# Kernel tuning notes

Hardware: AMD Instinct MI355X
Metric: run time of the kernel (lower is better)

Reference implementation:

```python
import jax, jax.numpy as jnp
import numpy as np
import math

D_MODEL = 2048
N_HEADS = 32
N_KV_HEADS = 8
HEAD_DIM = D_MODEL // N_HEADS  # 64
GROUPS = N_HEADS // N_KV_HEADS  # 4
WINDOW = 512


def setup_inputs() -> dict:
    key = jax.random.key(0)
    k0, k1, k2, k3, k4 = jax.random.split(key, 5)
    B, T = 1, 2048
    scale = 0.02
    return {
        "hidden_states": jax.random.normal(k0, (B, T, D_MODEL), dtype=jnp.float32),
        "Wq": jax.random.normal(k1, (D_MODEL, D_MODEL), dtype=jnp.float32) * scale,
        "Wk": jax.random.normal(k2, (N_KV_HEADS * HEAD_DIM, D_MODEL), dtype=jnp.float32) * scale,
        "Wv": jax.random.normal(k3, (N_KV_HEADS * HEAD_DIM, D_MODEL), dtype=jnp.float32) * scale,
        "Wo": jax.random.normal(k4, (D_MODEL, D_MODEL), dtype=jnp.float32) * scale,
    }


def _rope_tables(T, dim):
    # matches RotaryEmbedding: inv_freq over even indices, emb = cat(freqs, freqs)
    inv_freq = 1.0 / (10000.0 ** (jnp.arange(0, dim, 2, dtype=jnp.float32) / dim))
    freqs = jnp.arange(T, dtype=jnp.float32)[:, None] * inv_freq[None, :]  # [T, dim/2]
    emb = jnp.concatenate([freqs, freqs], axis=-1)  # [T, dim]
    return jnp.cos(emb), jnp.sin(emb)


def _rotate_half(x):
    d = x.shape[-1] // 2
    return jnp.concatenate([-x[..., d:], x[..., :d]], axis=-1)


def reference(hidden_states, Wq, Wk, Wv, Wo):
    B, T, _ = hidden_states.shape
    # projections (torch Linear: y = x @ W^T)
    q = (hidden_states @ Wq.T).reshape(B, T, N_HEADS, HEAD_DIM).transpose(0, 2, 1, 3)      # [B,H,T,D]
    k = (hidden_states @ Wk.T).reshape(B, T, N_KV_HEADS, HEAD_DIM).transpose(0, 2, 1, 3)   # [B,Hkv,T,D]
    v = (hidden_states @ Wv.T).reshape(B, T, N_KV_HEADS, HEAD_DIM).transpose(0, 2, 1, 3)
    # RoPE (cos/sin broadcast [T,D] over [B,H,T,D])
    cos, sin = _rope_tables(T, HEAD_DIM)
    q = q * cos + _rotate_half(q) * sin
    k = k * cos + _rotate_half(k) * sin
    # GQA: expand KV heads
    k = jnp.repeat(k, GROUPS, axis=1)  # [B,H,T,D]
    v = jnp.repeat(v, GROUPS, axis=1)
    scores = jnp.einsum('bhqd,bhkd->bhqk', q, k) / math.sqrt(HEAD_DIM)  # [B,H,T,T]
    if WINDOW < T:
        i = jnp.arange(T)[:, None]
        j = jnp.arange(T)[None, :]
        # row i keeps columns [max(0,i-W/2), min(T,i+W/2)) — same as the torch loop
        allowed = (j >= i - WINDOW // 2) & (j < i + WINDOW // 2)
        scores = jnp.where(allowed, scores, -jnp.inf)
    w = jax.nn.softmax(scores, axis=-1)
    out = jnp.einsum('bhqk,bhkd->bhqd', w, v)  # [B,H,T,D]
    out = out.transpose(0, 2, 1, 3).reshape(B, T, D_MODEL)
    return out @ Wo.T
```

## Files before the change

kernel.cpp:

```cpp
#include <hip/hip_runtime.h>
#include <math.h>

#define TLEN 2048
#define DMODEL 2048
#define NHEADS 32
#define NKV 8
#define HDIM 64
#define KVDIM 512
#define WHALF 256

typedef short shortx8 __attribute__((ext_vector_type(8)));
typedef float floatx4 __attribute__((ext_vector_type(4)));
typedef unsigned int uint32;

__device__ __forceinline__ unsigned short f2bf_rne(float x) {
    union { float f; uint32 u; } v; v.f = x;
    uint32 r = v.u + 0x7FFFu + ((v.u >> 16) & 1u);
    return (unsigned short)(r >> 16);
}

#define GL16(g, l)                                                              \
    __builtin_amdgcn_global_load_lds(                                           \
        (const __attribute__((address_space(1))) unsigned int*)(g),             \
        (__attribute__((address_space(3))) unsigned int*)(l), 16, 0, 0)

__global__ __launch_bounds__(256) void convert_inputs(const float* __restrict__ hs,
                                                      const float* __restrict__ Wq,
                                                      const float* __restrict__ Wk,
                                                      const float* __restrict__ Wv,
                                                      const float* __restrict__ Wo,
                                                      unsigned short* __restrict__ hsb,
                                                      unsigned short* __restrict__ Wcat,
                                                      unsigned short* __restrict__ Wob) {
    int b = blockIdx.x;
    const float* src; unsigned short* dst;
    if (b < 512)       { src = hs; dst = hsb; }
    else if (b < 1024) { src = Wq; dst = Wcat;                           b -= 512; }
    else if (b < 1152) { src = Wk; dst = Wcat + (size_t)2048 * DMODEL;   b -= 1024; }
    else if (b < 1280) { src = Wv; dst = Wcat + (size_t)2560 * DMODEL;   b -= 1152; }
    else               { src = Wo; dst = Wob;                            b -= 1280; }
    size_t base = (size_t)b * 8192 + threadIdx.x * 4;
#pragma unroll
    for (int it = 0; it < 8; ++it) {
        size_t off = base + (size_t)it * 1024;
        float4 v = *(const float4*)(src + off);
        short4 p;
        p.x = (short)f2bf_rne(v.x); p.y = (short)f2bf_rne(v.y);
        p.z = (short)f2bf_rne(v.z); p.w = (short)f2bf_rne(v.w);
        *(short4*)(dst + off) = p;
    }
}

__global__ __launch_bounds__(256) void gemm_qkv(const unsigned short* __restrict__ hsb,
                                                const unsigned short* __restrict__ Wcat,
                                                unsigned short* __restrict__ Qo,
                                                unsigned short* __restrict__ Ko,
                                                unsigned short* __restrict__ Vo) {
    __shared__ short Ah[128][128];
    __shared__ short Bh[64][128];

    const int bnx = blockIdx.x;
    int mode, coff;
    if (bnx < 32)      { mode = 0; coff = bnx * 64; }
    else if (bnx < 40) { mode = 1; coff = (bnx - 32) * 64; }
    else               { mode = 2; coff = (bnx - 40) * 64; }
    const unsigned short* Bbase = Wcat + (size_t)bnx * 64 * DMODEL;

    const int bm = blockIdx.y * 128;
    const int tid = threadIdx.x;
    const int w = tid >> 6, lane = tid & 63;
    const int wA = w * 32, wB = w * 16;
    const int lr = lane & 15, quad = lane >> 4;
    const int r4 = lane >> 4;

    const unsigned short* Ag[4];
    const unsigned short* Bg[4];
#pragma unroll
    for (int gm = 0; gm < 4; ++gm) {
        const int cof = ((lane & 15) ^ r4 ^ (gm << 2)) * 8;
        Ag[gm] = hsb   + (size_t)(bm + wA + 4 * gm + r4) * DMODEL + cof;
        Bg[gm] = Bbase + (size_t)(wB + 4 * gm + r4) * DMODEL + cof;
    }

    floatx4 acc[2][4];
#pragma unroll
    for (int i = 0; i < 2; ++i)
#pragma unroll
        for (int j = 0; j < 4; ++j) acc[i][j] = (floatx4)0.0f;

    for (int k0 = 0; k0 < DMODEL; k0 += 128) {
        __syncthreads();
#pragma unroll
        for (int q = 0; q < 2; ++q)
#pragma unroll
            for (int gm = 0; gm < 4; ++gm)
                GL16(Ag[gm] + (size_t)(16 * q) * DMODEL + k0, &Ah[wA + 16 * q + 4 * gm][0]);
#pragma unroll
        for (int gm = 0; gm < 4; ++gm)
            GL16(Bg[gm] + k0, &Bh[wB + 4 * gm][0]);
        __syncthreads();

#pragma unroll
        for (int s = 0; s < 4; ++s) {
            const int cs = ((s * 4 + quad) ^ lr) * 8;
            shortx8 a0 = *(shortx8*)&Ah[wA + lr][cs];
            shortx8 a1 = *(shortx8*)&Ah[wA + 16 + lr][cs];
            shortx8 bf[4];
#pragma unroll
            for (int j = 0; j < 4; ++j) bf[j] = *(shortx8*)&Bh[j * 16 + lr][cs];
#pragma unroll
            for (int j = 0; j < 4; ++j)
                acc[0][j] = __builtin_amdgcn_mfma_f32_16x16x32_bf16(a0, bf[j], acc[0][j], 0, 0, 0);
#pragma unroll
            for (int j = 0; j < 4; ++j)
                acc[1][j] = __builtin_amdgcn_mfma_f32_16x16x32_bf16(a1, bf[j], acc[1][j], 0, 0, 0);
        }
    }

    if (mode != 2) {
#pragma unroll
        for (int j = 0; j < 2; ++j) {
            float fr = exp2f(-(float)(j * 16 + lr) * (13.2877123795494f / 32.0f));
#pragma unroll
            for (int i = 0; i < 2; ++i) {
                const int row0 = bm + wA + i * 16 + quad * 4;
#pragma unroll
                for (int r = 0; r < 4; ++r) {
                    float s, c;
                    sincosf((float)(row0 + r) * fr, &s, &c);
                    float x1 = acc[i][j][r], x2 = acc[i][j + 2][r];
                    acc[i][j][r]     = x1 * c - x2 * s;
                    acc[i][j + 2][r] = x2 * c + x1 * s;
                }
            }
        }
    }

#pragma unroll
    for (int i = 0; i < 2; ++i) {
        const int row0 = bm + wA + i * 16 + quad * 4;
        if (mode == 0) {
#pragma unroll
            for (int j = 0; j < 4; ++j) {
                int col = coff + j * 16 + lr;
#pragma unroll
                for (int r = 0; r < 4; ++r)
                    Qo[(size_t)(row0 + r) * DMODEL + col] = f2bf_rne(0.125f * acc[i][j][r]);
            }
        } else if (mode == 1) {
#pragma unroll
            for (int j = 0; j < 4; ++j) {
                int col = coff + j * 16 + lr;
#pragma unroll
                for (int r = 0; r < 4; ++r)
                    Ko[(size_t)(row0 + r) * KVDIM + col] = f2bf_rne(acc[i][j][r]);
            }
        } else {
#pragma unroll
            for (int j = 0; j < 4; ++j) {
                int col = coff + j * 16 + lr;
                short4 pk;
                pk.x = (short)f2bf_rne(acc[i][j][0]);
                pk.y = (short)f2bf_rne(acc[i][j][1]);
                pk.z = (short)f2bf_rne(acc[i][j][2]);
                pk.w = (short)f2bf_rne(acc[i][j][3]);
                *(short4*)&Vo[(size_t)col * TLEN + row0] = pk;
            }
        }
    }
}

__global__ __launch_bounds__(512) void attn_mfma(const unsigned short* __restrict__ Qb,
                                                 const unsigned short* __restrict__ Kb,
                                                 const unsigned short* __restrict__ Vt,
                                                 unsigned short* __restrict__ Ab) {
    __shared__ short Qs[128][64];
    __shared__ short Ks[2][64][64];
    __shared__ short Vs[2][64][64];
    __shared__ short Ps[128][72];

    const int h = blockIdx.y, q0 = blockIdx.x * 128, kvh = h >> 2;
    const int tid = threadIdx.x;
    const int w = tid >> 6, lane = tid & 63;
    const int l15 = lane & 15, quad = lane >> 4;
    const int qw = q0 + w * 16;

    const int sr  = lane >> 3;
    const int sgc = ((lane & 7) ^ sr) * 8;

    int cb = q0 - WHALF; if (cb < 0) cb = 0;
    int ce = q0 + 128 + WHALF; if (ce > TLEN) ce = TLEN;

    const unsigned short* kbase = Kb + (size_t)(w * 8 + sr) * KVDIM + kvh * HDIM + sgc;
    const unsigned short* vbase = Vt + (size_t)(kvh * HDIM + w * 8 + sr) * TLEN + sgc;

    {
        const unsigned short* qsrc = Qb + (size_t)(qw + sr) * DMODEL + h * HDIM + sgc;
        GL16(qsrc,              &Qs[w * 16 + 0][0]);
        GL16(qsrc + 8 * DMODEL, &Qs[w * 16 + 8][0]);
        GL16(kbase + (size_t)cb * KVDIM, &Ks[0][w * 8][0]);
        GL16(vbase + cb,                 &Vs[0][w * 8][0]);
    }
    __syncthreads();

    shortx8 aq[2];
#pragma unroll
    for (int s = 0; s < 2; ++s) {
        const int cs = ((s * 4 + quad) ^ (l15 & 7)) * 8;
        aq[s] = *(shortx8*)&Qs[w * 16 + l15][cs];
    }

    floatx4 o[4];
#pragma unroll
    for (int j = 0; j < 4; ++j) o[j] = (floatx4)0.0f;
    float l_lane[4] = {0.0f, 0.0f, 0.0f, 0.0f};

    int p = 0;
    for (int ch0 = cb; ch0 < ce; ch0 += 64) {
        if (ch0 + 64 < ce) {
            GL16(kbase + (size_t)(ch0 + 64) * KVDIM, &Ks[p ^ 1][w * 8][0]);
            GL16(vbase + (ch0 + 64),                 &Vs[p ^ 1][w * 8][0]);
        }

        if (ch0 >= qw - 319 && ch0 <= qw + 270) {
            floatx4 sacc[4];
#pragma unroll
            for (int t = 0; t < 4; ++t) sacc[t] = (floatx4)0.0f;
#pragma unroll
            for (int s = 0; s < 2; ++s) {
                const int cs = ((s * 4 + quad) ^ (l15 & 7)) * 8;
#pragma unroll
                for (int t = 0; t < 4; ++t) {
                    shortx8 bk = *(shortx8*)&Ks[p][t * 16 + l15][cs];
                    sacc[t] = __builtin_amdgcn_mfma_f32_16x16x32_bf16(aq[s], bk, sacc[t], 0, 0, 0);
                }
            }

#pragma unroll
            for (int r = 0; r < 4; ++r) {
                const int q = qw + quad * 4 + r;
                const int prow = w * 16 + quad * 4 + r;
                const int rsw = (quad * 4 + r) & 7;
#pragma unroll
                for (int t = 0; t < 4; ++t) {
                    const int k = ch0 + t * 16 + l15;
                    bool valid = (k >= q - WHALF) && (k < q + WHALF);
                    float pv = valid ? __expf(sacc[t][r]) : 0.0f;
                    l_lane[r] += pv;
                    const int g = t * 2 + (l15 >> 3);
                    Ps[prow][((g ^ rsw) * 8) + (l15 & 7)] = (short)f2bf_rne(pv);
                }
            }

#pragma unroll
            for (int ks = 0; ks < 2; ++ks) {
                const int cs = ((ks * 4 + quad) ^ (l15 & 7)) * 8;
                const int pg = ((ks * 4 + quad) ^ (l15 & 7)) * 8;
                shortx8 ap = *(shortx8*)&Ps[w * 16 + l15][pg];
#pragma unroll
                for (int j = 0; j < 4; ++j) {
                    shortx8 bv = *(shortx8*)&Vs[p][j * 16 + l15][cs];
                    o[j] = __builtin_amdgcn_mfma_f32_16x16x32_bf16(ap, bv, o[j], 0, 0, 0);
                }
            }
        }

        __syncthreads();
        p ^= 1;
    }

#pragma unroll
    for (int r = 0; r < 4; ++r) {
        float l = l_lane[r];
#pragma unroll
        for (int mb = 1; mb < 16; mb <<= 1)
            l += __shfl_xor(l, mb, 64);
        float inv = 1.0f / l;
        const int q = qw + quad * 4 + r;
#pragma unroll
        for (int j = 0; j < 4; ++j)
            Ab[(size_t)q * DMODEL + h * HDIM + j * 16 + l15] = f2bf_rne(o[j][r] * inv);
    }
}

__global__ __launch_bounds__(256) void gemm_oproj(const unsigned short* __restrict__ Ab,
                                                  const unsigned short* __restrict__ Wob,
                                                  float* __restrict__ C) {
    __shared__ short Ah[128][128];
    __shared__ short Bh[64][128];

    const int bm = blockIdx.y * 128, bn = blockIdx.x * 64;
    const int tid = threadIdx.x;
    const int w = tid >> 6, lane = tid & 63;
    const int wA = w * 32, wB = w * 16;
    const int lr = lane & 15, quad = lane >> 4;
    const int r4 = lane >> 4;

    const unsigned short* Ag[4];
    const unsigned short* Bg[4];
#pragma unroll
    for (int gm = 0; gm < 4; ++gm) {
        const int cof = ((lane & 15) ^ r4 ^ (gm << 2)) * 8;
        Ag[gm] = Ab  + (size_t)(bm + wA + 4 * gm + r4) * DMODEL + cof;
        Bg[gm] = Wob + (size_t)(bn + wB + 4 * gm + r4) * DMODEL + cof;
    }

    floatx4 acc[2][4];
#pragma unroll
    for (int i = 0; i < 2; ++i)
#pragma unroll
        for (int j = 0; j < 4; ++j) acc[i][j] = (floatx4)0.0f;

    for (int k0 = 0; k0 < DMODEL; k0 += 128) {
        __syncthreads();
#pragma unroll
        for (int q = 0; q < 2; ++q)
#pragma unroll
            for (int gm = 0; gm < 4; ++gm)
                GL16(Ag[gm] + (size_t)(16 * q) * DMODEL + k0, &Ah[wA + 16 * q + 4 * gm][0]);
#pragma unroll
        for (int gm = 0; gm < 4; ++gm)
            GL16(Bg[gm] + k0, &Bh[wB + 4 * gm][0]);
        __syncthreads();

#pragma unroll
        for (int s = 0; s < 4; ++s) {
            const int cs = ((s * 4 + quad) ^ lr) * 8;
            shortx8 a0 = *(shortx8*)&Ah[wA + lr][cs];
            shortx8 a1 = *(shortx8*)&Ah[wA + 16 + lr][cs];
            shortx8 bf[4];
#pragma unroll
            for (int j = 0; j < 4; ++j) bf[j] = *(shortx8*)&Bh[j * 16 + lr][cs];
#pragma unroll
            for (int j = 0; j < 4; ++j)
                acc[0][j] = __builtin_amdgcn_mfma_f32_16x16x32_bf16(a0, bf[j], acc[0][j], 0, 0, 0);
#pragma unroll
            for (int j = 0; j < 4; ++j)
                acc[1][j] = __builtin_amdgcn_mfma_f32_16x16x32_bf16(a1, bf[j], acc[1][j], 0, 0, 0);
        }
    }

#pragma unroll
    for (int i = 0; i < 2; ++i) {
        const int row0 = bm + wA + i * 16 + quad * 4;
#pragma unroll
        for (int j = 0; j < 4; ++j) {
            int col = bn + j * 16 + lr;
#pragma unroll
            for (int r = 0; r < 4; ++r)
                C[(size_t)(row0 + r) * DMODEL + col] = acc[i][j][r];
        }
    }
}

extern "C" void kernel_launch(void* const* d_in, const int* in_sizes, int n_in,
                              void* d_out, int out_size, void* d_ws, size_t ws_size,
                              hipStream_t stream) {
    const float* hs = (const float*)d_in[0];
    const float* Wq = (const float*)d_in[1];
    const float* Wk = (const float*)d_in[2];
    const float* Wv = (const float*)d_in[3];
    const float* Wo = (const float*)d_in[4];
    float* out = (float*)d_out;

    unsigned short* Qb   = (unsigned short*)d_ws;
    unsigned short* Kb   = Qb + (size_t)TLEN * DMODEL;
    unsigned short* Vt   = Kb + (size_t)TLEN * KVDIM;
    unsigned short* hsAb = Vt + (size_t)KVDIM * TLEN;
    unsigned short* Wcat = hsAb + (size_t)TLEN * DMODEL;
    unsigned short* Wob  = Wcat + (size_t)3072 * DMODEL;

    dim3 blk(256);

    convert_inputs<<<1792, blk, 0, stream>>>(hs, Wq, Wk, Wv, Wo, hsAb, Wcat, Wob);

    gemm_qkv<<<dim3(48, TLEN / 128), blk, 0, stream>>>(hsAb, Wcat, Qb, Kb, Vt);

    attn_mfma<<<dim3(TLEN / 128, NHEADS), dim3(512), 0, stream>>>(Qb, Kb, Vt, hsAb);

    gemm_oproj<<<dim3(DMODEL / 64, TLEN / 128), blk, 0, stream>>>(hsAb, Wob, out);
}
```

Baseline: 181.8 us.

## Double-buffer LDS tiles in QKV and output-projection GEMMs with K=64 steps

Both projection GEMMs now keep two shared-memory stages of 64-wide K slices instead of one 128-wide slice. The next slice's global-to-LDS load is issued before computing on the current one, and only one barrier per iteration remains. The aim is to overlap global memory latency with MFMA work. LDS footprint stays the same, but the packing and swizzle of A/B rows into the half-width buffers is rewritten, which adds indexing complexity and some risk to correctness.

```diff
diff --git a/kernel.cpp b/kernel.cpp
--- a/kernel.cpp
+++ b/kernel.cpp
@@ -56,8 +56,8 @@
                                                 unsigned short* __restrict__ Qo,
                                                 unsigned short* __restrict__ Ko,
                                                 unsigned short* __restrict__ Vo) {
-    __shared__ short Ah[128][128];
-    __shared__ short Bh[64][128];
+    __shared__ short Ah[2][64][128];
+    __shared__ short Bh[2][32][128];
 
     const int bnx = blockIdx.x;
     int mode, coff;
@@ -69,17 +69,25 @@
     const int bm = blockIdx.y * 128;
     const int tid = threadIdx.x;
     const int w = tid >> 6, lane = tid & 63;
-    const int wA = w * 32, wB = w * 16;
+    const int wA = w * 32;
     const int lr = lane & 15, quad = lane >> 4;
-    const int r4 = lane >> 4;
-
+
+    const int pc = lane & 15, lq = lane >> 4;
     const unsigned short* Ag[4];
-    const unsigned short* Bg[4];
-#pragma unroll
-    for (int gm = 0; gm < 4; ++gm) {
-        const int cof = ((lane & 15) ^ r4 ^ (gm << 2)) * 8;
-        Ag[gm] = hsb   + (size_t)(bm + wA + 4 * gm + r4) * DMODEL + cof;
-        Bg[gm] = Bbase + (size_t)(wB + 4 * gm + r4) * DMODEL + cof;
+#pragma unroll
+    for (int g = 0; g < 4; ++g) {
+        const int ra4 = 4 * g + lq;
+        const int lc = pc ^ ra4;
+        const int m = w * 16 + ra4 + 64 * (lc >> 3);
+        Ag[g] = hsb + (size_t)(bm + m) * DMODEL + (lc & 7) * 8;
+    }
+    const unsigned short* Bg[2];
+#pragma unroll
+    for (int g = 0; g < 2; ++g) {
+        const int rb = w * 8 + 4 * g + lq;
+        const int lc = pc ^ (rb & 15);
+        const int n = rb + 32 * (lc >> 3);
+        Bg[g] = Bbase + (size_t)n * DMODEL + (lc & 7) * 8;
     }
 
     floatx4 acc[2][4];
@@ -88,33 +96,43 @@
 #pragma unroll
         for (int j = 0; j < 4; ++j) acc[i][j] = (floatx4)0.0f;
 
-    for (int k0 = 0; k0 < DMODEL; k0 += 128) {
+#pragma unroll
+    for (int g = 0; g < 4; ++g) GL16(Ag[g], &Ah[0][w * 16 + 4 * g][0]);
+#pragma unroll
+    for (int g = 0; g < 2; ++g) GL16(Bg[g], &Bh[0][w * 8 + 4 * g][0]);
+    __syncthreads();
+
+    for (int kt = 0; kt < 32; ++kt) {
+        const int p = kt & 1;
+        if (kt < 31) {
+            const int ko = (kt + 1) * 64;
+#pragma unroll
+            for (int g = 0; g < 4; ++g) GL16(Ag[g] + ko, &Ah[p ^ 1][w * 16 + 4 * g][0]);
+#pragma unroll
+            for (int g = 0; g < 2; ++g) GL16(Bg[g] + ko, &Bh[p ^ 1][w * 8 + 4 * g][0]);
+        }
+#pragma unroll
+        for (int s = 0; s < 2; ++s) {
+            shortx8 af[2], bf[4];
+#pragma unroll
+            for (int i = 0; i < 2; ++i) {
+                const int ha = (w * 2 + i) >> 2;
+                const int rowA = ((w * 32 + i * 16) & 63) + lr;
+                af[i] = *(shortx8*)&Ah[p][rowA][((ha * 8 + s * 4 + quad) ^ lr) * 8];
+            }
+#pragma unroll
+            for (int j = 0; j < 4; ++j) {
+                const int rowB = (j & 1) * 16 + lr;
+                bf[j] = *(shortx8*)&Bh[p][rowB][(((j >> 1) * 8 + s * 4 + quad) ^ lr) * 8];
+            }
+#pragma unroll
+            for (int j = 0; j < 4; ++j)
+                acc[0][j] = __builtin_amdgcn_mfma_f32_16x16x32_bf16(af[0], bf[j], acc[0][j], 0, 0, 0);
+#pragma unroll
+            for (int j = 0; j < 4; ++j)
+                acc[1][j] = __builtin_amdgcn_mfma_f32_16x16x32_bf16(af[1], bf[j], acc[1][j], 0, 0, 0);
+        }
         __syncthreads();
-#pragma unroll
-        for (int q = 0; q < 2; ++q)
-#pragma unroll
-            for (int gm = 0; gm < 4; ++gm)
-                GL16(Ag[gm] + (size_t)(16 * q) * DMODEL + k0, &Ah[wA + 16 * q + 4 * gm][0]);
-#pragma unroll
-        for (int gm = 0; gm < 4; ++gm)
-            GL16(Bg[gm] + k0, &Bh[wB + 4 * gm][0]);
-        __syncthreads();
-
-#pragma unroll
-        for (int s = 0; s < 4; ++s) {
-            const int cs = ((s * 4 + quad) ^ lr) * 8;
-            shortx8 a0 = *(shortx8*)&Ah[wA + lr][cs];
-            shortx8 a1 = *(shortx8*)&Ah[wA + 16 + lr][cs];
-            shortx8 bf[4];
-#pragma unroll
-            for (int j = 0; j < 4; ++j) bf[j] = *(shortx8*)&Bh[j * 16 + lr][cs];
-#pragma unroll
-            for (int j = 0; j < 4; ++j)
-                acc[0][j] = __builtin_amdgcn_mfma_f32_16x16x32_bf16(a0, bf[j], acc[0][j], 0, 0, 0);
-#pragma unroll
-            for (int j = 0; j < 4; ++j)
-                acc[1][j] = __builtin_amdgcn_mfma_f32_16x16x32_bf16(a1, bf[j], acc[1][j], 0, 0, 0);
-        }
     }
 
     if (mode != 2) {
@@ -286,23 +304,31 @@
 __global__ __launch_bounds__(256) void gemm_oproj(const unsigned short* __restrict__ Ab,
                                                   const unsigned short* __restrict__ Wob,
                                                   float* __restrict__ C) {
-    __shared__ short Ah[128][128];
-    __shared__ short Bh[64][128];
+    __shared__ short Ah[2][64][128];
+    __shared__ short Bh[2][32][128];
 
     const int bm = blockIdx.y * 128, bn = blockIdx.x * 64;
     const int tid = threadIdx.x;
     const int w = tid >> 6, lane = tid & 63;
-    const int wA = w * 32, wB = w * 16;
+    const int wA = w * 32;
     const int lr = lane & 15, quad = lane >> 4;
-    const int r4 = lane >> 4;
-
+
+    const int pc = lane & 15, lq = lane >> 4;
     const unsigned short* Ag[4];
-    const unsigned short* Bg[4];
-#pragma unroll
-    for (int gm = 0; gm < 4; ++gm) {
-        const int cof = ((lane & 15) ^ r4 ^ (gm << 2)) * 8;
-        Ag[gm] = Ab  + (size_t)(bm + wA + 4 * gm + r4) * DMODEL + cof;
-        Bg[gm] = Wob + (size_t)(bn + wB + 4 * gm + r4) * DMODEL + cof;
+#pragma unroll
+    for (int g = 0; g < 4; ++g) {
+        const int ra4 = 4 * g + lq;
+        const int lc = pc ^ ra4;
+        const int m = w * 16 + ra4 + 64 * (lc >> 3);
+        Ag[g] = Ab + (size_t)(bm + m) * DMODEL + (lc & 7) * 8;
+    }
+    const unsigned short* Bg[2];
+#pragma unroll
+    for (int g = 0; g < 2; ++g) {
+        const int rb = w * 8 + 4 * g + lq;
+        const int lc = pc ^ (rb & 15);
+        const int n = rb + 32 * (lc >> 3);
+        Bg[g] = Wob + (size_t)(bn + n) * DMODEL + (lc & 7) * 8;
     }
 
     floatx4 acc[2][4];
@@ -311,33 +337,43 @@
 #pragma unroll
         for (int j = 0; j < 4; ++j) acc[i][j] = (floatx4)0.0f;
 
-    for (int k0 = 0; k0 < DMODEL; k0 += 128) {
+#pragma unroll
+    for (int g = 0; g < 4; ++g) GL16(Ag[g], &Ah[0][w * 16 + 4 * g][0]);
+#pragma unroll
+    for (int g = 0; g < 2; ++g) GL16(Bg[g], &Bh[0][w * 8 + 4 * g][0]);
+    __syncthreads();
+
+    for (int kt = 0; kt < 32; ++kt) {
+        const int p = kt & 1;
+        if (kt < 31) {
+            const int ko = (kt + 1) * 64;
+#pragma unroll
+            for (int g = 0; g < 4; ++g) GL16(Ag[g] + ko, &Ah[p ^ 1][w * 16 + 4 * g][0]);
+#pragma unroll
+            for (int g = 0; g < 2; ++g) GL16(Bg[g] + ko, &Bh[p ^ 1][w * 8 + 4 * g][0]);
+        }
+#pragma unroll
+        for (int s = 0; s < 2; ++s) {
+            shortx8 af[2], bf[4];
+#pragma unroll
+            for (int i = 0; i < 2; ++i) {
+                const int ha = (w * 2 + i) >> 2;
+                const int rowA = ((w * 32 + i * 16) & 63) + lr;
+                af[i] = *(shortx8*)&Ah[p][rowA][((ha * 8 + s * 4 + quad) ^ lr) * 8];
+            }
+#pragma unroll
+            for (int j = 0; j < 4; ++j) {
+                const int rowB = (j & 1) * 16 + lr;
+                bf[j] = *(shortx8*)&Bh[p][rowB][(((j >> 1) * 8 + s * 4 + quad) ^ lr) * 8];
+            }
+#pragma unroll
+            for (int j = 0; j < 4; ++j)
+                acc[0][j] = __builtin_amdgcn_mfma_f32_16x16x32_bf16(af[0], bf[j], acc[0][j], 0, 0, 0);
+#pragma unroll
+            for (int j = 0; j < 4; ++j)
+                acc[1][j] = __builtin_amdgcn_mfma_f32_16x16x32_bf16(af[1], bf[j], acc[1][j], 0, 0, 0);
+        }
         __syncthreads();
-#pragma unroll
-        for (int q = 0; q < 2; ++q)
-#pragma unroll
-            for (int gm = 0; gm < 4; ++gm)
-                GL16(Ag[gm] + (size_t)(16 * q) * DMODEL + k0, &Ah[wA + 16 * q + 4 * gm][0]);
-#pragma unroll
-        for (int gm = 0; gm < 4; ++gm)
-            GL16(Bg[gm] + k0, &Bh[wB + 4 * gm][0]);
-        __syncthreads();
-
-#pragma unroll
-        for (int s = 0; s < 4; ++s) {
-            const int cs = ((s * 4 + quad) ^ lr) * 8;
-            shortx8 a0 = *(shortx8*)&Ah[wA + lr][cs];
-            shortx8 a1 = *(shortx8*)&Ah[wA + 16 + lr][cs];
-            shortx8 bf[4];
-#pragma unroll
-            for (int j = 0; j < 4; ++j) bf[j] = *(shortx8*)&Bh[j * 16 + lr][cs];
-#pragma unroll
-            for (int j = 0; j < 4; ++j)
-                acc[0][j] = __builtin_amdgcn_mfma_f32_16x16x32_bf16(a0, bf[j], acc[0][j], 0, 0, 0);
-#pragma unroll
-            for (int j = 0; j < 4; ++j)
-                acc[1][j] = __builtin_amdgcn_mfma_f32_16x16x32_bf16(a1, bf[j], acc[1][j], 0, 0, 0);
-        }
     }
 
 #pragma unroll
```

Result: slower. 187.1 us (+3.0%).
